# Kernel optimization log

Hardware: AMD Instinct MI355X
Metric: run time of the kernel (lower is better)

Reference implementation:

```python
import jax, jax.numpy as jnp
import numpy as np

DIM = 192
N_HEADS = 8
HEAD_DIM = DIM // N_HEADS
SCALE = 1.0 / np.sqrt(HEAD_DIM).astype(np.float32)
H_GRID, W_GRID = 32, 64
KH, KW = 7, 11


def build_local_mask():
    # Equivalent to the torch double-loop construction: token (h2,w2) may attend
    # to (h,w) iff |h2-h| <= KH//2 and |w2-w| <= KW//2 (odd kernels).
    hh = jnp.arange(H_GRID)
    ww = jnp.arange(W_GRID)
    dh_ok = jnp.abs(hh[:, None] - hh[None, :]) <= KH // 2  # [H, H]
    dw_ok = jnp.abs(ww[:, None] - ww[None, :]) <= KW // 2  # [W, W]
    allowed = dh_ok[:, None, :, None] & dw_ok[None, :, None, :]  # [H, W, H, W]
    allowed = allowed.reshape(H_GRID * W_GRID, H_GRID * W_GRID)
    return jnp.where(allowed, 0.0, -jnp.inf).astype(jnp.float32)  # [N, N]


def setup_inputs() -> dict:
    key = jax.random.key(0)
    ks = jax.random.split(key, 5)
    B, N = 4, H_GRID * W_GRID
    w_std = 1.0 / np.sqrt(DIM)
    x = jax.random.normal(ks[0], (B, N, DIM), dtype=jnp.float32)
    qkv_w = jax.random.normal(ks[1], (3 * DIM, DIM), dtype=jnp.float32) * w_std
    qkv_b = jax.random.normal(ks[2], (3 * DIM,), dtype=jnp.float32) * 0.02
    proj_w = jax.random.normal(ks[3], (DIM, DIM), dtype=jnp.float32) * w_std
    proj_b = jax.random.normal(ks[4], (DIM,), dtype=jnp.float32) * 0.02
    mask = build_local_mask()
    return {"x": x, "qkv_w": qkv_w, "qkv_b": qkv_b,
            "proj_w": proj_w, "proj_b": proj_b, "mask": mask}


def reference(x, qkv_w, qkv_b, proj_w, proj_b, mask):
    B, N, _ = x.shape
    qkv = x @ qkv_w.T + qkv_b                              # [B, N, 3*DIM]
    qkv = qkv.reshape(B, N, 3, N_HEADS, HEAD_DIM)
    qkv = jnp.transpose(qkv, (2, 0, 3, 1, 4))              # [3, B, h, N, d]
    q, k, v = qkv[0] * SCALE, qkv[1], qkv[2]
    attn = jnp.einsum('bhnd,bhmd->bhnm', q, k) + mask      # [B, h, N, N]
    attn = jax.nn.softmax(attn, axis=-1)                   # == log_softmax().exp()
    out = jnp.einsum('bhnm,bhmd->bhnd', attn, v)           # [B, h, N, d]
    out = jnp.transpose(out, (0, 2, 1, 3)).reshape(B, N, DIM)
    return out @ proj_w.T + proj_b
```

## Files before the change

kernel.cpp:

```cpp
#include <hip/hip_runtime.h>
#include <math.h>

#define H_GRID 32
#define W_GRID 64
#define NTOK   2048
#define NHEADS 8
#define HD     24
#define DIMC   192
#define BATCH  4

static constexpr float SCALE = 0.20412414523193154f;

typedef unsigned short ushort;
typedef unsigned int   uint;
typedef __attribute__((ext_vector_type(8))) _Float16 f16x8;
typedef __attribute__((ext_vector_type(4))) float    f32x4;

static __device__ __forceinline__ float4 ld4(const float* p) { return *(const float4*)p; }

static __device__ __forceinline__ ushort f2h(float f) {
    _Float16 h = (_Float16)f;
    union { _Float16 h; ushort u; } c; c.h = h; return c.u;
}
static __device__ __forceinline__ float h2f(ushort u) {
    union { ushort u; _Float16 h; } c; c.u = u; return (float)c.h;
}
static __device__ __forceinline__ f16x8 cvt8(float4 a, float4 b) {
    f16x8 r;
    r[0] = (_Float16)a.x; r[1] = (_Float16)a.y; r[2] = (_Float16)a.z; r[3] = (_Float16)a.w;
    r[4] = (_Float16)b.x; r[5] = (_Float16)b.y; r[6] = (_Float16)b.z; r[7] = (_Float16)b.w;
    return r;
}

__global__ __launch_bounds__(256, 4) void gemm_qkv(const float* __restrict__ x,
                                                   const float* __restrict__ Wf,
                                                   const float* __restrict__ bias,
                                                   ushort* __restrict__ Qh,
                                                   ushort* __restrict__ Kh,
                                                   ushort* __restrict__ VTh) {
    __shared__ ushort Ws[64 * 200];

    const int t    = threadIdx.x;
    const int wave = t >> 6, lane = t & 63;
    const int bx   = blockIdx.x;
    const int by   = blockIdx.y;
    const int m0   = bx * 64 + wave * 16;
    const int j0   = by * 64;
    const int n16  = lane & 15;
    const int kq   = lane >> 4;

    for (int i = t; i < 1536; i += 256) {
        const int r = i / 24, c = i - (i / 24) * 24;
        const float* wsrc = &Wf[(size_t)(j0 + r) * 192 + c * 8];
        const float4 w0 = ld4(wsrc), w1 = ld4(wsrc + 4);
        *(ushort4*)&Ws[r * 200 + c * 8] =
            make_ushort4(f2h(w0.x), f2h(w0.y), f2h(w0.z), f2h(w0.w));
        *(ushort4*)&Ws[r * 200 + c * 8 + 4] =
            make_ushort4(f2h(w1.x), f2h(w1.y), f2h(w1.z), f2h(w1.w));
    }

    if (by == 0) {
        for (int i = t; i < 1024; i += 256) {
            const int tok = bx * 64 + (i >> 4);
            const int h_  = (i >> 1) & 7;
            ushort* dst = (i & 1) ? Kh : Qh;
            const uint4 z = {0u, 0u, 0u, 0u};
            *(uint4*)&dst[((size_t)((tok >> 11) * 8 + h_) * 2048 + (tok & 2047)) * 32 + 24] = z;
        }
    }

    const float* ap = x + (size_t)(m0 + n16) * 192 + kq * 8;
    f16x8 af[6];
#pragma unroll
    for (int ks = 0; ks < 6; ks++) {
        const float4 a0 = ld4(ap + ks * 32);
        const float4 a1 = ld4(ap + ks * 32 + 4);
        af[ks] = cvt8(a0, a1);
    }

    f32x4 acc[4] = {f32x4{0,0,0,0}, f32x4{0,0,0,0}, f32x4{0,0,0,0}, f32x4{0,0,0,0}};

    __syncthreads();

#pragma unroll
    for (int ks = 0; ks < 6; ks++) {
#pragma unroll
        for (int nt = 0; nt < 4; nt++) {
            const f16x8 bf = *(const f16x8*)&Ws[(nt * 16 + n16) * 200 + kq * 8 + ks * 32];
            acc[nt] = __builtin_amdgcn_mfma_f32_16x16x32_f16(af[ks], bf, acc[nt], 0, 0, 0);
        }
    }

    const int band  = by / 3;
    const int mrow0 = m0 + kq * 4;
    const int b_    = mrow0 >> 11;
    const int tok0  = mrow0 & 2047;

    if (band == 2) {
#pragma unroll
        for (int nt = 0; nt < 4; nt++) {
            const int col = j0 + nt * 16 + n16;
            const int lc  = col - 384;
            const int h_  = lc / 24;
            const int d_  = lc - h_ * 24;
            const float bv = bias[col];
            ushort vv[4];
#pragma unroll
            for (int r = 0; r < 4; r++) vv[r] = f2h(acc[nt][r] + bv);
            const size_t addr = ((size_t)(b_ * 8 + h_) * 32 + d_) * 2080 + 8 + tok0;
            *(ushort4*)&VTh[addr] = make_ushort4(vv[0], vv[1], vv[2], vv[3]);
        }
    } else {
        const float sc_ = band ? 1.0f : SCALE;
        __syncthreads();
#pragma unroll
        for (int nt = 0; nt < 4; nt++) {
            const int col = j0 + nt * 16 + n16;
            const float bv = bias[col];
#pragma unroll
            for (int r = 0; r < 4; r++) {
                Ws[(wave * 16 + kq * 4 + r) * 68 + nt * 16 + n16] =
                    f2h((acc[nt][r] + bv) * sc_);
            }
        }
        __syncthreads();
        ushort* dst = band ? Kh : Qh;
        const int lc0 = j0 - band * 192;
#pragma unroll
        for (int it = 0; it < 4; it++) {
            const int item = t + 256 * it;
            const int tokl = item >> 4;
            const int cg   = item & 15;
            const ushort4 v = *(const ushort4*)&Ws[tokl * 68 + cg * 4];
            const int lc = lc0 + cg * 4;
            const int h_ = lc / 24;
            const int d0 = lc - h_ * 24;
            const int m  = bx * 64 + tokl;
            const size_t addr = ((size_t)((m >> 11) * 8 + h_) * 2048 + (m & 2047)) * 32 + d0;
            *(ushort4*)&dst[addr] = v;
        }
    }
}

__global__ __launch_bounds__(256, 4) void attn_mfma(const ushort* __restrict__ Qh,
                                                    const ushort* __restrict__ Kh,
                                                    const ushort* __restrict__ VTh,
                                                    ushort* __restrict__ aws) {
    const int id    = blockIdx.x;
    const int head  = id & 7;
    const int qtile = (id >> 3) & 63;
    const int b     = id >> 9;
    const int qh0   = (qtile >> 3) * 4;
    const int qw0   = (qtile & 7) * 8;
    const int kw0a  = qw0 - 8;

    const int t = threadIdx.x;
    const int w = t >> 6, lane = t & 63;
    const int n16 = lane & 15, quad = lane >> 4;
    const int bh = b * 8 + head;

    __shared__ ushort P[32 * 328];
    __shared__ ushort Os[32 * 28];
    __shared__ float  mxbuf[64], sumbuf[64];

    const ushort* Qb = Qh + (size_t)bh * 65536;
    const ushort* Kb = Kh + (size_t)bh * 65536;

    const int mt = w >> 1, nth = w & 1;
    const int mrow = 16 * mt + n16;
    const int tq_a = ((qh0 + (mrow >> 3)) << 6) + qw0 + (mrow & 7);
    const f16x8 qf = *(const f16x8*)&Qb[(size_t)tq_a * 32 + quad * 8];

    float sv[10][4];
    float mx4[4] = {-3e38f, -3e38f, -3e38f, -3e38f};
#pragma unroll
    for (int half = 0; half < 2; half++) {
        f16x8 kf[5];
        int khvv[5], kwvv[5];
#pragma unroll
        for (int jj = 0; jj < 5; jj++) {
            const int j = half * 5 + jj;
            const int slot = (nth * 10 + j) * 16 + n16;
            const int rr = slot >> 5, cc = slot & 31;
            khvv[jj] = qh0 - 3 + rr;
            kwvv[jj] = kw0a + cc;
            const int tok = (min(max(khvv[jj], 0), 31) << 6) + min(max(kwvv[jj], 0), 63);
            kf[jj] = *(const f16x8*)&Kb[(size_t)tok * 32 + quad * 8];
        }
#pragma unroll
        for (int jj = 0; jj < 5; jj++) {
            const int j = half * 5 + jj;
            f32x4 a = f32x4{0, 0, 0, 0};
            a = __builtin_amdgcn_mfma_f32_16x16x32_f16(qf, kf[jj], a, 0, 0, 0);
            const int khv = khvv[jj], kwv = kwvv[jj];
            const bool kok = (khv >= 0) && (khv < 32) && (kwv >= 0) && (kwv < 64);
#pragma unroll
            for (int r = 0; r < 4; r++) {
                const int m   = 16 * mt + quad * 4 + r;
                const int qhv = qh0 + (m >> 3);
                const int qwv = qw0 + (m & 7);
                const bool valid = kok && (abs(khv - qhv) <= 3) && (abs(kwv - qwv) <= 5);
                const float s = valid ? a[r] : -3e38f;
                sv[j][r] = s;
                mx4[r] = fmaxf(mx4[r], s);
            }
        }
    }
#pragma unroll
    for (int d = 1; d < 16; d <<= 1)
#pragma unroll
        for (int r = 0; r < 4; r++) mx4[r] = fmaxf(mx4[r], __shfl_xor(mx4[r], d));
    if (n16 == 0) {
#pragma unroll
        for (int r = 0; r < 4; r++) mxbuf[w * 16 + quad * 4 + r] = mx4[r];
    }
    __syncthreads();
#pragma unroll
    for (int r = 0; r < 4; r++) mx4[r] = fmaxf(mx4[r], mxbuf[(w ^ 1) * 16 + quad * 4 + r]);

    float sum4[4] = {0.f, 0.f, 0.f, 0.f};
#pragma unroll
    for (int j = 0; j < 10; j++) {
        const int slot = (nth * 10 + j) * 16 + n16;
#pragma unroll
        for (int r = 0; r < 4; r++) {
            const float p = __expf(sv[j][r] - mx4[r]);
            const ushort ph = f2h(p);
            sum4[r] += h2f(ph);
            P[(16 * mt + quad * 4 + r) * 328 + slot] = ph;
        }
    }
#pragma unroll
    for (int d = 1; d < 16; d <<= 1)
#pragma unroll
        for (int r = 0; r < 4; r++) sum4[r] += __shfl_xor(sum4[r], d);
    if (n16 == 0) {
#pragma unroll
        for (int r = 0; r < 4; r++) sumbuf[w * 16 + quad * 4 + r] = sum4[r];
    }
    __syncthreads();

    const int mtP = w >> 1, ntP = w & 1;
    const int dcol = 16 * ntP + n16;
    const ushort* VTb = VTh + (size_t)bh * 66560;
    f32x4 acc = f32x4{0, 0, 0, 0};
#pragma unroll
    for (int half = 0; half < 2; half++) {
        f16x8 vf[5], pa[5];
#pragma unroll
        for (int kk = 0; kk < 5; kk++) {
            const int ks = half * 5 + kk;
            const int kh_cl = min(max(qh0 - 3 + ks, 0), 31);
            vf[kk] = *(const f16x8*)&VTb[(size_t)dcol * 2080 + 8 + (kh_cl << 6) + kw0a + quad * 8];
            pa[kk] = *(const f16x8*)&P[(16 * mtP + n16) * 328 + ks * 32 + quad * 8];
        }
#pragma unroll
        for (int kk = 0; kk < 5; kk++) {
            acc = __builtin_amdgcn_mfma_f32_16x16x32_f16(pa[kk], vf[kk], acc, 0, 0, 0);
        }
    }
    if (dcol < 24) {
#pragma unroll
        for (int r = 0; r < 4; r++) {
            const int m = 16 * mtP + quad * 4 + r;
            const float tot = sumbuf[(2 * mtP) * 16 + (m & 15)] +
                              sumbuf[(2 * mtP + 1) * 16 + (m & 15)];
            Os[m * 28 + dcol] = f2h(acc[r] / tot);
        }
    }
    __syncthreads();

    if (t < 192) {
        const int tok = t / 6, g = t - (t / 6) * 6;
        const ushort4 v = *(const ushort4*)&Os[tok * 28 + g * 4];
        const int tq = ((qh0 + (tok >> 3)) << 6) + qw0 + (tok & 7);
        *(ushort4*)&aws[((size_t)(b * 2048 + tq)) * 192 + head * 24 + g * 4] = v;
    }
}

__global__ __launch_bounds__(128, 4) void gemm_proj(const ushort* __restrict__ Ah,
                                                    const float* __restrict__ Wf,
                                                    const float* __restrict__ bias,
                                                    float* __restrict__ C) {
    __shared__ ushort Ws[64 * 200];

    const int t    = threadIdx.x;
    const int wave = t >> 6, lane = t & 63;
    const int m0   = blockIdx.x * 32 + wave * 16;
    const int j0   = blockIdx.y * 64;
    const int n16  = lane & 15;
    const int kq   = lane >> 4;

    for (int i = t; i < 1536; i += 128) {
        const int r = i / 24, c = i - (i / 24) * 24;
        const float* wsrc = &Wf[(size_t)(j0 + r) * 192 + c * 8];
        const float4 w0 = ld4(wsrc), w1 = ld4(wsrc + 4);
        *(ushort4*)&Ws[r * 200 + c * 8] =
            make_ushort4(f2h(w0.x), f2h(w0.y), f2h(w0.z), f2h(w0.w));
        *(ushort4*)&Ws[r * 200 + c * 8 + 4] =
            make_ushort4(f2h(w1.x), f2h(w1.y), f2h(w1.z), f2h(w1.w));
    }

    const ushort* ap = Ah + (size_t)(m0 + n16) * 192 + kq * 8;

    f16x8 af[6];
#pragma unroll
    for (int ks = 0; ks < 6; ks++) af[ks] = *(const f16x8*)(ap + ks * 32);

    f32x4 acc[4] = {f32x4{0,0,0,0}, f32x4{0,0,0,0}, f32x4{0,0,0,0}, f32x4{0,0,0,0}};

    __syncthreads();

#pragma unroll
    for (int ks = 0; ks < 6; ks++) {
#pragma unroll
        for (int nt = 0; nt < 4; nt++) {
            const f16x8 bf = *(const f16x8*)&Ws[(nt * 16 + n16) * 200 + kq * 8 + ks * 32];
            acc[nt] = __builtin_amdgcn_mfma_f32_16x16x32_f16(af[ks], bf, acc[nt], 0, 0, 0);
        }
    }

#pragma unroll
    for (int nt = 0; nt < 4; nt++) {
        const int col = j0 + nt * 16 + n16;
        const float bv = bias[col];
#pragma unroll
        for (int r = 0; r < 4; r++) {
            const int m = m0 + kq * 4 + r;
            C[(size_t)m * 192 + col] = acc[nt][r] + bv;
        }
    }
}

extern "C" void kernel_launch(void* const* d_in, const int* in_sizes, int n_in,
                              void* d_out, int out_size, void* d_ws, size_t ws_size,
                              hipStream_t stream) {
    const float* x      = (const float*)d_in[0];
    const float* qkv_w  = (const float*)d_in[1];
    const float* qkv_b  = (const float*)d_in[2];
    const float* proj_w = (const float*)d_in[3];
    const float* proj_b = (const float*)d_in[4];

    char* wsb = (char*)d_ws;
    ushort* Qh   = (ushort*)(wsb + 0);
    ushort* Kh   = (ushort*)(wsb + 4194304);
    ushort* VTh  = (ushort*)(wsb + 8388608);
    ushort* awsh = (ushort*)(wsb + 12648448);
    float*  out  = (float*)d_out;

    hipLaunchKernelGGL(gemm_qkv, dim3(128, 9), dim3(256), 0, stream,
                       x, qkv_w, qkv_b, Qh, Kh, VTh);
    hipLaunchKernelGGL(attn_mfma, dim3(2048), dim3(256), 0, stream,
                       Qh, Kh, VTh, awsh);
    hipLaunchKernelGGL(gemm_proj, dim3(256, 3), dim3(128), 0, stream,
                       awsh, proj_w, proj_b, out);
}
```

Before: 110.5 us.

## Double row tiles per block in GEMMs and streamline attention mask and epilogue

Both GEMM kernels now have each wave compute two 16-row tiles against the same shared-memory weight tile. Each block covers 128 rows, so the grids shrink and the per-block weight fp32-to-fp16 conversion is amortized over twice the work. The attention kernel precomputes the local-window validity bits into a 64-bit mask. It also writes its normalized output straight to global memory using a reciprocal, dropping the Os shared staging buffer and a barrier. The trade-offs are higher register pressure, fewer blocks to fill the GPU, and scattered 2-byte global stores in the attention epilogue.

```diff
diff --git a/kernel.cpp b/kernel.cpp
--- a/kernel.cpp
+++ b/kernel.cpp
@@ -44,10 +44,11 @@
     const int wave = t >> 6, lane = t & 63;
     const int bx   = blockIdx.x;
     const int by   = blockIdx.y;
-    const int m0   = bx * 64 + wave * 16;
     const int j0   = by * 64;
     const int n16  = lane & 15;
     const int kq   = lane >> 4;
+    const int mA   = bx * 128 + wave * 16;
+    const int mB   = mA + 64;
 
     for (int i = t; i < 1536; i += 256) {
         const int r = i / 24, c = i - (i / 24) * 24;
@@ -60,8 +61,8 @@
     }
 
     if (by == 0) {
-        for (int i = t; i < 1024; i += 256) {
-            const int tok = bx * 64 + (i >> 4);
+        for (int i = t; i < 2048; i += 256) {
+            const int tok = bx * 128 + (i >> 4);
             const int h_  = (i >> 1) & 7;
             ushort* dst = (i & 1) ? Kh : Qh;
             const uint4 z = {0u, 0u, 0u, 0u};
@@ -69,16 +70,17 @@
         }
     }
 
-    const float* ap = x + (size_t)(m0 + n16) * 192 + kq * 8;
-    f16x8 af[6];
+    const float* apA = x + (size_t)(mA + n16) * 192 + kq * 8;
+    const float* apB = apA + 64 * 192;
+    f16x8 afA[6], afB[6];
 #pragma unroll
     for (int ks = 0; ks < 6; ks++) {
-        const float4 a0 = ld4(ap + ks * 32);
-        const float4 a1 = ld4(ap + ks * 32 + 4);
-        af[ks] = cvt8(a0, a1);
-    }
-
-    f32x4 acc[4] = {f32x4{0,0,0,0}, f32x4{0,0,0,0}, f32x4{0,0,0,0}, f32x4{0,0,0,0}};
+        afA[ks] = cvt8(ld4(apA + ks * 32), ld4(apA + ks * 32 + 4));
+        afB[ks] = cvt8(ld4(apB + ks * 32), ld4(apB + ks * 32 + 4));
+    }
+
+    f32x4 accA[4] = {f32x4{0,0,0,0}, f32x4{0,0,0,0}, f32x4{0,0,0,0}, f32x4{0,0,0,0}};
+    f32x4 accB[4] = {f32x4{0,0,0,0}, f32x4{0,0,0,0}, f32x4{0,0,0,0}, f32x4{0,0,0,0}};
 
     __syncthreads();
 
@@ -87,16 +89,15 @@
 #pragma unroll
         for (int nt = 0; nt < 4; nt++) {
             const f16x8 bf = *(const f16x8*)&Ws[(nt * 16 + n16) * 200 + kq * 8 + ks * 32];
-            acc[nt] = __builtin_amdgcn_mfma_f32_16x16x32_f16(af[ks], bf, acc[nt], 0, 0, 0);
-        }
-    }
-
-    const int band  = by / 3;
-    const int mrow0 = m0 + kq * 4;
-    const int b_    = mrow0 >> 11;
-    const int tok0  = mrow0 & 2047;
+            accA[nt] = __builtin_amdgcn_mfma_f32_16x16x32_f16(afA[ks], bf, accA[nt], 0, 0, 0);
+            accB[nt] = __builtin_amdgcn_mfma_f32_16x16x32_f16(afB[ks], bf, accB[nt], 0, 0, 0);
+        }
+    }
+
+    const int band = by / 3;
 
     if (band == 2) {
+        const int rowA = mA + kq * 4, rowB = mB + kq * 4;
 #pragma unroll
         for (int nt = 0; nt < 4; nt++) {
             const int col = j0 + nt * 16 + n16;
@@ -104,11 +105,16 @@
             const int h_  = lc / 24;
             const int d_  = lc - h_ * 24;
             const float bv = bias[col];
-            ushort vv[4];
-#pragma unroll
-            for (int r = 0; r < 4; r++) vv[r] = f2h(acc[nt][r] + bv);
-            const size_t addr = ((size_t)(b_ * 8 + h_) * 32 + d_) * 2080 + 8 + tok0;
-            *(ushort4*)&VTh[addr] = make_ushort4(vv[0], vv[1], vv[2], vv[3]);
+            ushort vvA[4], vvB[4];
+#pragma unroll
+            for (int r = 0; r < 4; r++) {
+                vvA[r] = f2h(accA[nt][r] + bv);
+                vvB[r] = f2h(accB[nt][r] + bv);
+            }
+            const size_t baseA = ((size_t)((rowA >> 11) * 8 + h_) * 32 + d_) * 2080 + 8 + (rowA & 2047);
+            const size_t baseB = ((size_t)((rowB >> 11) * 8 + h_) * 32 + d_) * 2080 + 8 + (rowB & 2047);
+            *(ushort4*)&VTh[baseA] = make_ushort4(vvA[0], vvA[1], vvA[2], vvA[3]);
+            *(ushort4*)&VTh[baseB] = make_ushort4(vvB[0], vvB[1], vvB[2], vvB[3]);
         }
     } else {
         const float sc_ = band ? 1.0f : SCALE;
@@ -120,14 +126,16 @@
 #pragma unroll
             for (int r = 0; r < 4; r++) {
                 Ws[(wave * 16 + kq * 4 + r) * 68 + nt * 16 + n16] =
-                    f2h((acc[nt][r] + bv) * sc_);
+                    f2h((accA[nt][r] + bv) * sc_);
+                Ws[(64 + wave * 16 + kq * 4 + r) * 68 + nt * 16 + n16] =
+                    f2h((accB[nt][r] + bv) * sc_);
             }
         }
         __syncthreads();
         ushort* dst = band ? Kh : Qh;
         const int lc0 = j0 - band * 192;
 #pragma unroll
-        for (int it = 0; it < 4; it++) {
+        for (int it = 0; it < 8; it++) {
             const int item = t + 256 * it;
             const int tokl = item >> 4;
             const int cg   = item & 15;
@@ -135,7 +143,7 @@
             const int lc = lc0 + cg * 4;
             const int h_ = lc / 24;
             const int d0 = lc - h_ * 24;
-            const int m  = bx * 64 + tokl;
+            const int m  = bx * 128 + tokl;
             const size_t addr = ((size_t)((m >> 11) * 8 + h_) * 2048 + (m & 2047)) * 32 + d0;
             *(ushort4*)&dst[addr] = v;
         }
@@ -160,13 +168,27 @@
     const int bh = b * 8 + head;
 
     __shared__ ushort P[32 * 328];
-    __shared__ ushort Os[32 * 28];
     __shared__ float  mxbuf[64], sumbuf[64];
 
     const ushort* Qb = Qh + (size_t)bh * 65536;
     const ushort* Kb = Kh + (size_t)bh * 65536;
 
     const int mt = w >> 1, nth = w & 1;
+
+    unsigned long long imask = 0ull;
+#pragma unroll
+    for (int j = 0; j < 10; j++) {
+        const int slot = (nth * 10 + j) * 16 + n16;
+        const int rr = slot >> 5, cc = slot & 31;
+#pragma unroll
+        for (int r = 0; r < 4; r++) {
+            const int m  = 16 * mt + quad * 4 + r;
+            const int dh = rr - 3 - (m >> 3);
+            const int dw = cc - 8 - (m & 7);
+            if (abs(dh) <= 3 && abs(dw) <= 5) imask |= 1ull << (j * 4 + r);
+        }
+    }
+
     const int mrow = 16 * mt + n16;
     const int tq_a = ((qh0 + (mrow >> 3)) << 6) + qw0 + (mrow & 7);
     const f16x8 qf = *(const f16x8*)&Qb[(size_t)tq_a * 32 + quad * 8];
@@ -196,10 +218,7 @@
             const bool kok = (khv >= 0) && (khv < 32) && (kwv >= 0) && (kwv < 64);
 #pragma unroll
             for (int r = 0; r < 4; r++) {
-                const int m   = 16 * mt + quad * 4 + r;
-                const int qhv = qh0 + (m >> 3);
-                const int qwv = qw0 + (m & 7);
-                const bool valid = kok && (abs(khv - qhv) <= 3) && (abs(kwv - qwv) <= 5);
+                const bool valid = kok && ((imask >> (j * 4 + r)) & 1);
                 const float s = valid ? a[r] : -3e38f;
                 sv[j][r] = s;
                 mx4[r] = fmaxf(mx4[r], s);
@@ -259,26 +278,21 @@
             acc = __builtin_amdgcn_mfma_f32_16x16x32_f16(pa[kk], vf[kk], acc, 0, 0, 0);
         }
     }
+
     if (dcol < 24) {
 #pragma unroll
         for (int r = 0; r < 4; r++) {
             const int m = 16 * mtP + quad * 4 + r;
-            const float tot = sumbuf[(2 * mtP) * 16 + (m & 15)] +
-                              sumbuf[(2 * mtP + 1) * 16 + (m & 15)];
-            Os[m * 28 + dcol] = f2h(acc[r] / tot);
-        }
-    }
-    __syncthreads();
-
-    if (t < 192) {
-        const int tok = t / 6, g = t - (t / 6) * 6;
-        const ushort4 v = *(const ushort4*)&Os[tok * 28 + g * 4];
-        const int tq = ((qh0 + (tok >> 3)) << 6) + qw0 + (tok & 7);
-        *(ushort4*)&aws[((size_t)(b * 2048 + tq)) * 192 + head * 24 + g * 4] = v;
-    }
-}
-
-__global__ __launch_bounds__(128, 4) void gemm_proj(const ushort* __restrict__ Ah,
+            const float tot = sumbuf[(2 * mtP) * 16 + quad * 4 + r] +
+                              sumbuf[(2 * mtP + 1) * 16 + quad * 4 + r];
+            const float rt = __builtin_amdgcn_rcpf(tot);
+            const int tq = ((qh0 + (m >> 3)) << 6) + qw0 + (m & 7);
+            aws[((size_t)(b * 2048 + tq)) * 192 + head * 24 + dcol] = f2h(acc[r] * rt);
+        }
+    }
+}
+
+__global__ __launch_bounds__(256, 4) void gemm_proj(const ushort* __restrict__ Ah,
                                                     const float* __restrict__ Wf,
                                                     const float* __restrict__ bias,
                                                     float* __restrict__ C) {
@@ -286,12 +300,13 @@
 
     const int t    = threadIdx.x;
     const int wave = t >> 6, lane = t & 63;
-    const int m0   = blockIdx.x * 32 + wave * 16;
     const int j0   = blockIdx.y * 64;
     const int n16  = lane & 15;
     const int kq   = lane >> 4;
-
-    for (int i = t; i < 1536; i += 128) {
+    const int mA   = blockIdx.x * 128 + wave * 16;
+    const int mB   = mA + 64;
+
+    for (int i = t; i < 1536; i += 256) {
         const int r = i / 24, c = i - (i / 24) * 24;
         const float* wsrc = &Wf[(size_t)(j0 + r) * 192 + c * 8];
         const float4 w0 = ld4(wsrc), w1 = ld4(wsrc + 4);
@@ -301,13 +316,18 @@
             make_ushort4(f2h(w1.x), f2h(w1.y), f2h(w1.z), f2h(w1.w));
     }
 
-    const ushort* ap = Ah + (size_t)(m0 + n16) * 192 + kq * 8;
-
-    f16x8 af[6];
-#pragma unroll
-    for (int ks = 0; ks < 6; ks++) af[ks] = *(const f16x8*)(ap + ks * 32);
-
-    f32x4 acc[4] = {f32x4{0,0,0,0}, f32x4{0,0,0,0}, f32x4{0,0,0,0}, f32x4{0,0,0,0}};
+    const ushort* apA = Ah + (size_t)(mA + n16) * 192 + kq * 8;
+    const ushort* apB = apA + 64 * 192;
+
+    f16x8 afA[6], afB[6];
+#pragma unroll
+    for (int ks = 0; ks < 6; ks++) {
+        afA[ks] = *(const f16x8*)(apA + ks * 32);
+        afB[ks] = *(const f16x8*)(apB + ks * 32);
+    }
+
+    f32x4 accA[4] = {f32x4{0,0,0,0}, f32x4{0,0,0,0}, f32x4{0,0,0,0}, f32x4{0,0,0,0}};
+    f32x4 accB[4] = {f32x4{0,0,0,0}, f32x4{0,0,0,0}, f32x4{0,0,0,0}, f32x4{0,0,0,0}};
 
     __syncthreads();
 
@@ -316,7 +336,8 @@
 #pragma unroll
         for (int nt = 0; nt < 4; nt++) {
             const f16x8 bf = *(const f16x8*)&Ws[(nt * 16 + n16) * 200 + kq * 8 + ks * 32];
-            acc[nt] = __builtin_amdgcn_mfma_f32_16x16x32_f16(af[ks], bf, acc[nt], 0, 0, 0);
+            accA[nt] = __builtin_amdgcn_mfma_f32_16x16x32_f16(afA[ks], bf, accA[nt], 0, 0, 0);
+            accB[nt] = __builtin_amdgcn_mfma_f32_16x16x32_f16(afB[ks], bf, accB[nt], 0, 0, 0);
         }
     }
 
@@ -326,8 +347,8 @@
         const float bv = bias[col];
 #pragma unroll
         for (int r = 0; r < 4; r++) {
-            const int m = m0 + kq * 4 + r;
-            C[(size_t)m * 192 + col] = acc[nt][r] + bv;
+            C[(size_t)(mA + kq * 4 + r) * 192 + col] = accA[nt][r] + bv;
+            C[(size_t)(mB + kq * 4 + r) * 192 + col] = accB[nt][r] + bv;
         }
     }
 }
@@ -348,10 +369,10 @@
     ushort* awsh = (ushort*)(wsb + 12648448);
     float*  out  = (float*)d_out;
 
-    hipLaunchKernelGGL(gemm_qkv, dim3(128, 9), dim3(256), 0, stream,
+    hipLaunchKernelGGL(gemm_qkv, dim3(64, 9), dim3(256), 0, stream,
                        x, qkv_w, qkv_b, Qh, Kh, VTh);
     hipLaunchKernelGGL(attn_mfma, dim3(2048), dim3(256), 0, stream,
                        Qh, Kh, VTh, awsh);
-    hipLaunchKernelGGL(gemm_proj, dim3(256, 3), dim3(128), 0, stream,
+    hipLaunchKernelGGL(gemm_proj, dim3(64, 3), dim3(256), 0, stream,
                        awsh, proj_w, proj_b, out);
 }
```

After: 113.1 us. 2.3% more time.
